# Optimization experiments

Measured on AMD Instinct MI355X. Metric: run time of the kernel, lower is better.

## Reference

```python
import jax, jax.numpy as jnp
import numpy as np

N_QUBITS = 10
N_LAYERS = 2
BATCH = 4096


def _apply_1q(state, U, w):
    # state: (B, 2,...,2); apply 2x2 gate U on wire w (axis 1+w)
    s = jnp.moveaxis(state, 1 + w, -1)
    s = s @ U.T
    return jnp.moveaxis(s, -1, 1 + w)


def _apply_cnot(state, c, t):
    # flip target axis where control axis == 1
    s = jnp.moveaxis(state, (1 + c, 1 + t), (-2, -1))
    s = jnp.stack([s[..., 0, :], s[..., 1, ::-1]], axis=-2)
    return jnp.moveaxis(s, (-2, -1), (1 + c, 1 + t))


def _simulate(x, weights):
    B, n = x.shape
    n_layers = weights.shape[0]
    # AngleEmbedding rotation='Y': RY(x_i)|0> = [cos(x_i/2), sin(x_i/2)] per qubit
    half = x * 0.5
    c, s = jnp.cos(half), jnp.sin(half)
    state = jnp.ones((B, 1), jnp.complex64)
    for w in range(n):
        q = jnp.stack([c[:, w], s[:, w]], axis=-1).astype(jnp.complex64)  # (B,2)
        state = (state[:, :, None] * q[:, None, :]).reshape(B, -1)
    state = state.reshape((B,) + (2,) * n)
    # BasicEntanglerLayers: per layer RX(weights[l,w]) on each wire, then CNOT ring
    cnot_pairs = [(0, 1)] if n == 2 else [(i, (i + 1) % n) for i in range(n)]
    for l in range(n_layers):
        for w in range(n):
            th = weights[l, w] * 0.5
            cw = jnp.cos(th).astype(jnp.complex64)
            sw = (-1j * jnp.sin(th)).astype(jnp.complex64)
            U = jnp.stack([jnp.stack([cw, sw]), jnp.stack([sw, cw])])  # RX
            state = _apply_1q(state, U, w)
        for (cq, tq) in cnot_pairs:
            state = _apply_cnot(state, cq, tq)
    # PauliZ expvals: marginal prob(bit_i=0) - prob(bit_i=1)
    probs = state.real**2 + state.imag**2  # (B,2,...,2)
    zs = []
    for i in range(n):
        axes = tuple(a for a in range(1, n + 1) if a != 1 + i)
        p = probs.sum(axis=axes)  # (B,2)
        zs.append(p[:, 0] - p[:, 1])
    return jnp.stack(zs, axis=-1).astype(jnp.float32)  # (B, n)


def setup_inputs() -> dict:
    key = jax.random.key(0)
    k1, k2 = jax.random.split(key)
    x = jax.random.uniform(k1, (BATCH, N_QUBITS), jnp.float32, -1.0, 1.0)  # tanh-bounded
    bound = 1.0 / np.sqrt(N_QUBITS)
    weights = jax.random.uniform(k2, (N_LAYERS, N_QUBITS), jnp.float32, -bound, bound)
    return {"x": x, "weights": weights}


def reference(x, weights):
    return _simulate(x, weights)
```

## Files before the change

### kernel.cpp

```cpp
#include <hip/hip_runtime.h>


template<int DL, int DLN>
__device__ __forceinline__ void apply_gate(float (&ar)[16], float (&ai)[16],
                                           float c, float s) {
  float nr[16], ni[16];
#pragma unroll
  for (int r = 0; r < 16; ++r) {
    float pr, pi;
    if constexpr (DLN == 0) {
      pr = ar[r ^ DL];
      pi = ai[r ^ DL];
    } else {
      pr = __shfl_xor(ar[r ^ DL], DLN);
      pi = __shfl_xor(ai[r ^ DL], DLN);
    }
    nr[r] = fmaf(s, pi, c * ar[r]);
    ni[r] = fmaf(-s, pr, c * ai[r]);
  }
#pragma unroll
  for (int r = 0; r < 16; ++r) { ar[r] = nr[r]; ai[r] = ni[r]; }
}

__global__ void __launch_bounds__(256)
qsim_kernel(const float* __restrict__ x, const float* __restrict__ wts,
            float* __restrict__ out, int B) {
  const int lane = threadIdx.x & 63;
  const int b = blockIdx.x * 4 + (threadIdx.x >> 6);
  if (b >= B) return;

  float qr0[10], qi0[10], qr1[10], qi1[10], c2[10], s2[10];
  const float* xb = x + b * 10;
#pragma unroll
  for (int w = 0; w < 10; ++w) {
    float xh = 0.5f * xb[w];
    float t1 = 0.5f * wts[w];
    float t2 = 0.5f * wts[10 + w];
    float cx = __cosf(xh), sx = __sinf(xh);
    float c1 = __cosf(t1), s1 = __sinf(t1);
    c2[w] = __cosf(t2);
    s2[w] = __sinf(t2);
    qr0[w] = c1 * cx;  qi0[w] = -s1 * sx;
    qr1[w] = c1 * sx;  qi1[w] = -s1 * cx;
  }

  float Pr = 1.0f, Pi = 0.0f;
#pragma unroll
  for (int w = 4; w < 10; ++w) {
    int bit = (lane >> (w - 4)) & 1;
    float qr = bit ? qr1[w] : qr0[w];
    float qi = bit ? qi1[w] : qi0[w];
    float nr = Pr * qr - Pi * qi;
    float ni = Pr * qi + Pi * qr;
    Pr = nr; Pi = ni;
  }

  float ar[16], ai[16];
  ar[0] = Pr; ai[0] = Pi;
#pragma unroll
  for (int w = 0; w < 4; ++w) {
#pragma unroll
    for (int r = 0; r < 8; ++r) {
      if (r < (1 << w)) {
        float lr = ar[r], li = ai[r];
        ar[r + (1 << w)] = lr * qr1[w] - li * qi1[w];
        ai[r + (1 << w)] = lr * qi1[w] + li * qr1[w];
        ar[r] = lr * qr0[w] - li * qi0[w];
        ai[r] = lr * qi0[w] + li * qr0[w];
      }
    }
  }

  apply_gate<3, 0>(ar, ai, c2[0], s2[0]);
  apply_gate<6, 0>(ar, ai, c2[1], s2[1]);
  apply_gate<12, 0>(ar, ai, c2[2], s2[2]);
  apply_gate<8, 1>(ar, ai, c2[3], s2[3]);
  apply_gate<0, 3>(ar, ai, c2[4], s2[4]);
  apply_gate<0, 6>(ar, ai, c2[5], s2[5]);
  apply_gate<0, 12>(ar, ai, c2[6], s2[6]);
  apply_gate<0, 24>(ar, ai, c2[7], s2[7]);
  apply_gate<0, 48>(ar, ai, c2[8], s2[8]);
  apply_gate<3, 32>(ar, ai, c2[9], s2[9]);

  float p[16];
#pragma unroll
  for (int r = 0; r < 16; ++r) p[r] = ar[r] * ar[r] + ai[r] * ai[r];
#pragma unroll
  for (int stp = 0; stp < 4; ++stp) {
    const int st = 1 << stp;
#pragma unroll
    for (int r = 0; r < 16; ++r) {
      if (!(r & st)) {
        float a0 = p[r], a1 = p[r | st];
        p[r] = a0 + a1;
        p[r | st] = a0 - a1;
      }
    }
  }

  constexpr int G[10] = {0x2AB, 0x3FD, 0x3FA, 0x3F5, 0x3EA,
                         0x3D5, 0x3AA, 0x355, 0x2AA, 0x155};
  float outv = 0.0f;
#pragma unroll
  for (int i = 0; i < 10; ++i) {
    float v = p[G[i] & 15];
    int par = __popc(lane & (G[i] >> 4)) & 1;
    v = par ? -v : v;
#pragma unroll
    for (int k = 1; k < 64; k <<= 1) v += __shfl_xor(v, k);
    if (lane == i) outv = v;
  }
  if (lane < 10) out[b * 10 + lane] = outv;
}

extern "C" void kernel_launch(void* const* d_in, const int* in_sizes, int n_in,
                              void* d_out, int out_size, void* d_ws, size_t ws_size,
                              hipStream_t stream) {
  const float* x = (const float*)d_in[0];
  const float* wts = (const float*)d_in[1];
  float* out = (float*)d_out;
  const int B = in_sizes[0] / 10;
  const int blocks = (B + 3) / 4;
  qsim_kernel<<<blocks, 256, 0, stream>>>(x, wts, out, B);
}
```

Baseline: 68.46 us.

## Use DPP/swizzle lane exchanges and a lane Walsh-Hadamard transform for the final reduction

Replaces most __shfl_xor cross-lane exchanges in the gate application with DPP quad permutes and ds_swizzle patterns, which avoid the LDS-backed bpermute path. The ten per-output butterfly reductions become four in-lane Walsh-Hadamard transforms across the wavefront, whose results are written from specific lanes that hold each parity pattern. Trig setup is moved next to its use to lower register pressure. This relies on the swizzle and DPP patterns matching the XOR masks and on hardcoded lane/output mappings that are easy to get wrong.

```diff
diff --git a/kernel.cpp b/kernel.cpp
--- a/kernel.cpp
+++ b/kernel.cpp
@@ -1,5 +1,30 @@
 #include <hip/hip_runtime.h>
 
+
+template<int CTRL>
+__device__ __forceinline__ float dppf(float v) {
+  int i = __builtin_bit_cast(int, v);
+  i = __builtin_amdgcn_update_dpp(i, i, CTRL, 0xF, 0xF, false);
+  return __builtin_bit_cast(float, i);
+}
+template<int PAT>
+__device__ __forceinline__ float swzf(float v) {
+  int i = __builtin_bit_cast(int, v);
+  i = __builtin_amdgcn_ds_swizzle(i, PAT);
+  return __builtin_bit_cast(float, i);
+}
+
+template<int DL, int DLN>
+__device__ __forceinline__ float fetchp(const float (&a)[16], int r) {
+  float v = a[r ^ DL];
+  if constexpr (DLN == 0)       return v;
+  else if constexpr (DLN == 1)  return dppf<0xB1>(v);
+  else if constexpr (DLN == 3)  return dppf<0x1B>(v);
+  else if constexpr (DLN == 6)  return swzf<0x181F>(v);
+  else if constexpr (DLN == 12) return swzf<0x301F>(v);
+  else if constexpr (DLN == 24) return swzf<0x601F>(v);
+  else                          return __shfl_xor(v, DLN);
+}
 
 template<int DL, int DLN>
 __device__ __forceinline__ void apply_gate(float (&ar)[16], float (&ai)[16],
@@ -7,19 +32,24 @@
   float nr[16], ni[16];
 #pragma unroll
   for (int r = 0; r < 16; ++r) {
-    float pr, pi;
-    if constexpr (DLN == 0) {
-      pr = ar[r ^ DL];
-      pi = ai[r ^ DL];
-    } else {
-      pr = __shfl_xor(ar[r ^ DL], DLN);
-      pi = __shfl_xor(ai[r ^ DL], DLN);
-    }
+    float pr = fetchp<DL, DLN>(ar, r);
+    float pi = fetchp<DL, DLN>(ai, r);
     nr[r] = fmaf(s, pi, c * ar[r]);
     ni[r] = fmaf(-s, pr, c * ai[r]);
   }
 #pragma unroll
   for (int r = 0; r < 16; ++r) { ar[r] = nr[r]; ai[r] = ni[r]; }
+}
+
+__device__ __forceinline__ float lane_wht(float v, float g1, float g2, float g4,
+                                          float g8, float g16, float g32) {
+  v = fmaf(g1,  v, dppf<0xB1>(v));
+  v = fmaf(g2,  v, dppf<0x4E>(v));
+  v = fmaf(g4,  v, swzf<0x101F>(v));
+  v = fmaf(g8,  v, swzf<0x201F>(v));
+  v = fmaf(g16, v, swzf<0x401F>(v));
+  v = fmaf(g32, v, __shfl_xor(v, 32));
+  return v;
 }
 
 __global__ void __launch_bounds__(256)
@@ -28,28 +58,18 @@
   const int lane = threadIdx.x & 63;
   const int b = blockIdx.x * 4 + (threadIdx.x >> 6);
   if (b >= B) return;
-
-  float qr0[10], qi0[10], qr1[10], qi1[10], c2[10], s2[10];
   const float* xb = x + b * 10;
-#pragma unroll
-  for (int w = 0; w < 10; ++w) {
-    float xh = 0.5f * xb[w];
-    float t1 = 0.5f * wts[w];
-    float t2 = 0.5f * wts[10 + w];
-    float cx = __cosf(xh), sx = __sinf(xh);
-    float c1 = __cosf(t1), s1 = __sinf(t1);
-    c2[w] = __cosf(t2);
-    s2[w] = __sinf(t2);
-    qr0[w] = c1 * cx;  qi0[w] = -s1 * sx;
-    qr1[w] = c1 * sx;  qi1[w] = -s1 * cx;
-  }
 
   float Pr = 1.0f, Pi = 0.0f;
 #pragma unroll
   for (int w = 4; w < 10; ++w) {
+    float xh = 0.5f * xb[w];
+    float t1 = 0.5f * wts[w];
+    float cx = __cosf(xh), sx = __sinf(xh);
+    float c1 = __cosf(t1), s1w = __sinf(t1);
     int bit = (lane >> (w - 4)) & 1;
-    float qr = bit ? qr1[w] : qr0[w];
-    float qi = bit ? qi1[w] : qi0[w];
+    float qr = c1 * (bit ? sx : cx);
+    float qi = -s1w * (bit ? cx : sx);
     float nr = Pr * qr - Pi * qi;
     float ni = Pr * qi + Pi * qr;
     Pr = nr; Pi = ni;
@@ -59,28 +79,42 @@
   ar[0] = Pr; ai[0] = Pi;
 #pragma unroll
   for (int w = 0; w < 4; ++w) {
+    float xh = 0.5f * xb[w];
+    float t1 = 0.5f * wts[w];
+    float cx = __cosf(xh), sx = __sinf(xh);
+    float c1 = __cosf(t1), s1w = __sinf(t1);
+    float q0r = c1 * cx, q0i = -s1w * sx;
+    float q1r = c1 * sx, q1i = -s1w * cx;
 #pragma unroll
     for (int r = 0; r < 8; ++r) {
       if (r < (1 << w)) {
         float lr = ar[r], li = ai[r];
-        ar[r + (1 << w)] = lr * qr1[w] - li * qi1[w];
-        ai[r + (1 << w)] = lr * qi1[w] + li * qr1[w];
-        ar[r] = lr * qr0[w] - li * qi0[w];
-        ai[r] = lr * qi0[w] + li * qr0[w];
+        ar[r + (1 << w)] = lr * q1r - li * q1i;
+        ai[r + (1 << w)] = lr * q1i + li * q1r;
+        ar[r] = lr * q0r - li * q0i;
+        ai[r] = lr * q0i + li * q0r;
       }
     }
   }
 
-  apply_gate<3, 0>(ar, ai, c2[0], s2[0]);
-  apply_gate<6, 0>(ar, ai, c2[1], s2[1]);
-  apply_gate<12, 0>(ar, ai, c2[2], s2[2]);
-  apply_gate<8, 1>(ar, ai, c2[3], s2[3]);
-  apply_gate<0, 3>(ar, ai, c2[4], s2[4]);
-  apply_gate<0, 6>(ar, ai, c2[5], s2[5]);
-  apply_gate<0, 12>(ar, ai, c2[6], s2[6]);
-  apply_gate<0, 24>(ar, ai, c2[7], s2[7]);
-  apply_gate<0, 48>(ar, ai, c2[8], s2[8]);
-  apply_gate<3, 32>(ar, ai, c2[9], s2[9]);
+  float c2[10], s2v[10];
+#pragma unroll
+  for (int w = 0; w < 10; ++w) {
+    float t2 = 0.5f * wts[10 + w];
+    c2[w] = __cosf(t2);
+    s2v[w] = __sinf(t2);
+  }
+
+  apply_gate<3, 0>(ar, ai, c2[0], s2v[0]);
+  apply_gate<6, 0>(ar, ai, c2[1], s2v[1]);
+  apply_gate<12, 0>(ar, ai, c2[2], s2v[2]);
+  apply_gate<8, 1>(ar, ai, c2[3], s2v[3]);
+  apply_gate<0, 3>(ar, ai, c2[4], s2v[4]);
+  apply_gate<0, 6>(ar, ai, c2[5], s2v[5]);
+  apply_gate<0, 12>(ar, ai, c2[6], s2v[6]);
+  apply_gate<0, 24>(ar, ai, c2[7], s2v[7]);
+  apply_gate<0, 48>(ar, ai, c2[8], s2v[8]);
+  apply_gate<3, 32>(ar, ai, c2[9], s2v[9]);
 
   float p[16];
 #pragma unroll
@@ -98,19 +132,25 @@
     }
   }
 
-  constexpr int G[10] = {0x2AB, 0x3FD, 0x3FA, 0x3F5, 0x3EA,
-                         0x3D5, 0x3AA, 0x355, 0x2AA, 0x155};
-  float outv = 0.0f;
-#pragma unroll
-  for (int i = 0; i < 10; ++i) {
-    float v = p[G[i] & 15];
-    int par = __popc(lane & (G[i] >> 4)) & 1;
-    v = par ? -v : v;
-#pragma unroll
-    for (int k = 1; k < 64; k <<= 1) v += __shfl_xor(v, k);
-    if (lane == i) outv = v;
-  }
-  if (lane < 10) out[b * 10 + lane] = outv;
+  const float g1  = (lane & 1)  ? -1.0f : 1.0f;
+  const float g2  = (lane & 2)  ? -1.0f : 1.0f;
+  const float g4  = (lane & 4)  ? -1.0f : 1.0f;
+  const float g8  = (lane & 8)  ? -1.0f : 1.0f;
+  const float g16 = (lane & 16) ? -1.0f : 1.0f;
+  const float g32 = (lane & 32) ? -1.0f : 1.0f;
+  float w5  = lane_wht(p[5],  g1, g2, g4, g8, g16, g32);
+  float w10 = lane_wht(p[10], g1, g2, g4, g8, g16, g32);
+  float w11 = lane_wht(p[11], g1, g2, g4, g8, g16, g32);
+  float w13 = lane_wht(p[13], g1, g2, g4, g8, g16, g32);
+
+  float* ob = out + b * 10;
+  if (lane == 42) { ob[0] = w11; ob[8] = w10; }
+  if (lane == 63) { ob[1] = w13; ob[2] = w10; ob[3] = w5; }
+  if (lane == 62) { ob[4] = w10; }
+  if (lane == 61) { ob[5] = w5; }
+  if (lane == 58) { ob[6] = w10; }
+  if (lane == 53) { ob[7] = w5; }
+  if (lane == 21) { ob[9] = w5; }
 }
 
 extern "C" void kernel_launch(void* const* d_in, const int* in_sizes, int n_in,
```

Measured after the change: 62.71 us. 8.4% less time.
